# Performance work log

Measured on AMD Instinct MI355X. Metric: run time of the kernel, lower is better.

## Reference

```python
import jax, jax.numpy as jnp
import numpy as np
import math

B, C, H, W = 2, 256, 40, 40
NH, DK, DV, ERF = 8, 32, 32, 5
PAD = (ERF - 1) // 2
STRIDE = 2
HB, WB = 2 * H, 2 * W  # bottom (finer) level spatial size


def _unfold(x, k, p, s):
    # faithful torch F.unfold: x [B,C,Hi,Wi] -> [B, C*k*k, L], channel layout (c, kh, kw)
    Bn, Ci, Hi, Wi = x.shape
    xp = jnp.pad(x, ((0, 0), (0, 0), (p, p), (p, p)))
    Ho = (Hi + 2 * p - k) // s + 1
    Wo = (Wi + 2 * p - k) // s + 1
    rows = (jnp.arange(Ho) * s)[:, None] + jnp.arange(k)[None, :]  # [Ho,k]
    cols = (jnp.arange(Wo) * s)[:, None] + jnp.arange(k)[None, :]  # [Wo,k]
    pat = xp[:, :, rows[:, :, None, None], cols[None, None, :, :]]  # [B,C,Ho,k,Wo,k]
    pat = pat.transpose(0, 1, 3, 5, 2, 4)  # [B,C,k,k,Ho,Wo]
    return pat.reshape(Bn, Ci * k * k, Ho * Wo)


def _fold(y, out_hw, k, p, s):
    # faithful torch F.fold (scatter-add of overlapping patches)
    Bn, Ck2, L = y.shape
    Ci = Ck2 // (k * k)
    Hout, Wout = out_hw
    Ho = (Hout + 2 * p - k) // s + 1
    Wo = (Wout + 2 * p - k) // s + 1
    pat = y.reshape(Bn, Ci, k, k, Ho, Wo).transpose(0, 1, 4, 2, 5, 3)  # [B,C,Ho,k,Wo,k]
    rows = (jnp.arange(Ho) * s)[:, None] + jnp.arange(k)[None, :]
    cols = (jnp.arange(Wo) * s)[:, None] + jnp.arange(k)[None, :]
    out = jnp.zeros((Bn, Ci, Hout + 2 * p, Wout + 2 * p), y.dtype)
    out = out.at[:, :, rows[:, :, None, None], cols[None, None, :, :]].add(pat)
    return out[:, :, p:p + Hout, p:p + Wout]


def _conv1x1(x, w):
    # 1x1 conv, no bias; w [Cout, Cin]
    return jnp.einsum('oc,bchw->bohw', w, x)


def _plan_forward(top, bot, w_tk, w_tq, w_tv, w_bk, w_bq, w_bv, w_tf, w_bf):
    Bsz = top.shape[0]
    Hb, Wb = bot.shape[2], bot.shape[3]
    Bn = Bsz * NH  # heads merged into batch (head-major channel split)

    def top_proj(w, d):
        y = _conv1x1(top, w).reshape(Bn, d, H, W)
        return y.transpose(0, 2, 3, 1).reshape(Bn * H * W, 1, d)

    def bot_proj(w, d):
        y = _conv1x1(bot, w).reshape(Bn, d, Hb, Wb)
        u = _unfold(y, ERF, PAD, STRIDE)  # [Bn, d*e^2, H*W]
        # NOTE: original code reshapes (d*e^2) -> (e^2, d) directly, mixing
        # channel/position layout; we replicate that exactly.
        return u.transpose(0, 2, 1).reshape(Bn * H * W, ERF * ERF, d)

    K = jnp.concatenate([top_proj(w_tk, DK), bot_proj(w_bk, DK)], axis=1)  # [N,n,dk]
    Q = jnp.concatenate([top_proj(w_tq, DK), bot_proj(w_bq, DK)], axis=1)
    V = jnp.concatenate([top_proj(w_tv, DV), bot_proj(w_bv, DV)], axis=1)  # [N,n,dv]

    # weight[i,j] = key_i . query_j / sqrt(dk)  (no softmax)
    att = jnp.einsum('nid,njd->nij', K, Q) / math.sqrt(DK)
    out = jnp.einsum('nij,njv->niv', att, V)  # [N, n, dv]

    top_ret = out[:, 0, :].reshape(Bn, H, W, DV).transpose(0, 3, 1, 2)
    top_ret = top_ret.reshape(Bsz, NH * DV, H, W)

    bot_flat = out[:, 1:, :].reshape(Bn, H * W, ERF * ERF * DV).transpose(0, 2, 1)
    bot_ret = _fold(bot_flat, (Hb, Wb), ERF, PAD, STRIDE)  # [Bn, DV, Hb, Wb]
    bot_ret = bot_ret.reshape(Bsz, NH * DV, Hb, Wb)

    return _conv1x1(top_ret, w_tf), _conv1x1(bot_ret, w_bf)


def setup_inputs() -> dict:
    key = jax.random.key(0)
    ks = jax.random.split(key, 10)
    std = 0.01
    return {
        'top_feat': jax.random.normal(ks[0], (B, C, H, W), jnp.float32),
        'bot_feat': jax.random.normal(ks[1], (B, C, HB, WB), jnp.float32),
        'w_top_key': jax.random.normal(ks[2], (NH * DK, C), jnp.float32) * std,
        'w_top_query': jax.random.normal(ks[3], (NH * DK, C), jnp.float32) * std,
        'w_top_value': jax.random.normal(ks[4], (NH * DV, C), jnp.float32) * std,
        'w_bot_key': jax.random.normal(ks[5], (NH * DK, C), jnp.float32) * std,
        'w_bot_query': jax.random.normal(ks[6], (NH * DK, C), jnp.float32) * std,
        'w_bot_value': jax.random.normal(ks[7], (NH * DV, C), jnp.float32) * std,
        'w_top_fuse': jax.random.normal(ks[8], (C, NH * DV), jnp.float32) * std,
        'w_bot_fuse': jax.random.normal(ks[9], (C, NH * DV), jnp.float32) * std,
    }


def reference(top_feat, bot_feat, w_top_key, w_top_query, w_top_value,
              w_bot_key, w_bot_query, w_bot_value, w_top_fuse, w_bot_fuse):
    return _plan_forward(top_feat, bot_feat, w_top_key, w_top_query, w_top_value,
                         w_bot_key, w_bot_query, w_bot_value, w_top_fuse, w_bot_fuse)
```

## Files before the change

kernel.cpp:

```cpp
#include <hip/hip_runtime.h>

#define NB    2
#define NCH   256
#define HH    40
#define WW    40
#define HWT   1600
#define HBs   80
#define WBs   80
#define HWB   6400
#define NHD   8
#define BN    16

#define OFF_PTOP 0
#define OFF_PBOT 2457600
#define OFF_TR   12288000
#define OFF_BA   13107200
#define OFF_ATT  16384000
#define WS_NEED_DENSE  (36864000ULL * 4ULL)

__global__ __launch_bounds__(256) void proj_gemm(
    const float* __restrict__ X,
    const float* __restrict__ Wk,
    const float* __restrict__ Wq,
    const float* __restrict__ Wv,
    float* __restrict__ P,
    int npos)
{
  __shared__ float As[16][64];
  __shared__ float Bs[16][64];
  const int tid  = threadIdx.x;
  const int b    = blockIdx.z;
  const int oc0  = blockIdx.y * 64;
  const int pos0 = blockIdx.x * 64;
  const int tx   = tid & 15;
  const int ty   = tid >> 4;
  const int kqv  = oc0 >> 8;
  const int ocr  = oc0 & 255;
  const float* Wsel = (kqv == 0) ? Wk : ((kqv == 1) ? Wq : Wv);
  const float* Xb   = X + (size_t)b * NCH * npos;

  const int la_r = tid >> 2;
  const int la_c = (tid & 3) * 4;
  const int lb_r = tid >> 4;
  const int lb_c = (tid & 15) * 4;

  float acc[4][4];
#pragma unroll
  for (int i = 0; i < 4; ++i)
#pragma unroll
    for (int j = 0; j < 4; ++j) acc[i][j] = 0.f;

  for (int kt = 0; kt < 256; kt += 16) {
    float4 av = *(const float4*)&Wsel[(size_t)(ocr + la_r) * 256 + kt + la_c];
    float4 bv = *(const float4*)&Xb[(size_t)(kt + lb_r) * npos + pos0 + lb_c];
    __syncthreads();
    As[la_c + 0][la_r] = av.x;
    As[la_c + 1][la_r] = av.y;
    As[la_c + 2][la_r] = av.z;
    As[la_c + 3][la_r] = av.w;
    *(float4*)&Bs[lb_r][lb_c] = bv;
    __syncthreads();
#pragma unroll
    for (int kk = 0; kk < 16; ++kk) {
      float a[4], bb[4];
      *(float4*)a  = *(const float4*)&As[kk][tx * 4];
      *(float4*)bb = *(const float4*)&Bs[kk][ty * 4];
#pragma unroll
      for (int i = 0; i < 4; ++i)
#pragma unroll
        for (int j = 0; j < 4; ++j) acc[i][j] += a[i] * bb[j];
    }
  }

  const int ocl  = oc0 + tx * 4;
  const int hd   = ocl & 255;
  const int head = hd >> 5;
  const int d0   = hd & 31;
  const int bh   = b * NHD + head;
  float* Pb = P + (size_t)(kqv * BN + bh) * npos * 32;
#pragma unroll
  for (int j = 0; j < 4; ++j) {
    const int pos = pos0 + ty * 4 + j;
    *(float4*)&Pb[(size_t)pos * 32 + d0] =
        make_float4(acc[0][j], acc[1][j], acc[2][j], acc[3][j]);
  }
}

__device__ __forceinline__ void stage_rows(
    float* dst,
    const float* __restrict__ Ptopr,
    const float* __restrict__ Pbotp,
    int ho, int wo, int v, float scl)
{
  dst[v] = Ptopr[v] * scl;
#pragma unroll
  for (int p = 0; p < 25; ++p) {
    const int ki = p / 5, kj = p % 5;
    const int hb = 2 * ho - 2 + ki;
    const int wb = 2 * wo - 2 + kj;
    float val = 0.f;
    if (hb >= 0 && hb < HBs && wb >= 0 && wb < WBs)
      val = Pbotp[(size_t)(hb * WBs + wb) * 32 + v] * scl;
    dst[32 + v * 25 + p] = val;
  }
}

__global__ __launch_bounds__(256, 3) void attn_dense(
    const float* __restrict__ Ptop,
    const float* __restrict__ Pbot,
    float* __restrict__ TR,
    float* __restrict__ AttOut)
{
  __shared__ float SQ[8][832];
  __shared__ float SV[8][832];

  const int tid  = threadIdx.x;
  const int widx = tid >> 6;
  const int lane = tid & 63;
  const int nsub = lane >> 5;
  const int v    = lane & 31;
  const int slot = widx * 2 + nsub;
  const int n    = (blockIdx.x * 4 + widx) * 2 + nsub;
  const int b    = n / (NHD * HWT);
  const int head = (n / HWT) % NHD;
  const int hw   = n % HWT;
  const int ho   = hw / WW, wo = hw % WW;
  const int bh   = b * NHD + head;
  const float scale = 0.17677669529663687f;

  float* SQs = &SQ[slot][0];
  float* SVs = &SV[slot][0];

  stage_rows(SQs, Ptop + ((size_t)(1 * BN + bh) * HWT + hw) * 32,
             Pbot + (size_t)(1 * BN + bh) * HWB * 32, ho, wo, v, scale);
  stage_rows(SVs, Ptop + ((size_t)(2 * BN + bh) * HWT + hw) * 32,
             Pbot + (size_t)(2 * BN + bh) * HWB * 32, ho, wo, v, 1.f);

  float m[32];
#pragma unroll
  for (int x = 0; x < 32; ++x) m[x] = 0.f;

#pragma unroll 2
  for (int j = 0; j < 26; ++j) {
    const float vv = SVs[j * 32 + v];
    const float* qr = &SQs[j * 32];
#pragma unroll
    for (int c = 0; c < 8; ++c) {
      float4 t = *(const float4*)&qr[c * 4];
      m[c * 4 + 0] += t.x * vv;
      m[c * 4 + 1] += t.y * vv;
      m[c * 4 + 2] += t.z * vv;
      m[c * 4 + 3] += t.w * vv;
    }
  }

  stage_rows(SQs, Ptop + ((size_t)(0 * BN + bh) * HWT + hw) * 32,
             Pbot + (size_t)(0 * BN + bh) * HWB * 32, ho, wo, v, 1.f);

  float* TRn = TR + ((size_t)(b * HWT + hw)) * 256 + head * 32;
#pragma unroll 2
  for (int i = 0; i < 26; ++i) {
    const float* kr = &SQs[i * 32];
    float s0 = 0.f, s1 = 0.f, s2 = 0.f, s3 = 0.f;
#pragma unroll
    for (int c = 0; c < 8; ++c) {
      float4 t = *(const float4*)&kr[c * 4];
      s0 += t.x * m[c * 4 + 0];
      s1 += t.y * m[c * 4 + 1];
      s2 += t.z * m[c * 4 + 2];
      s3 += t.w * m[c * 4 + 3];
    }
    const float o = (s0 + s1) + (s2 + s3);
    if (i == 0) TRn[v] = o;
    else        SVs[(i - 1) * 32 + v] = o;
  }

  float* AOn = AttOut + (size_t)n * 800;
#pragma unroll 5
  for (int j = 0; j < 25; ++j)
    AOn[j * 32 + v] = SVs[v * 25 + j];
}

__global__ __launch_bounds__(256) void fold_gather(
    const float* __restrict__ AttOut,
    float* __restrict__ BA)
{
  const int t    = blockIdx.x * 256 + threadIdx.x;
  const int dq   = (t & 7) * 4;
  const int head = (t >> 3) & 7;
  const int pw   = t >> 6;
  const int pix  = pw % HWB;
  const int b    = pw / HWB;
  const int hb   = pix / WBs, wb = pix % WBs;

  const float* A = AttOut + (size_t)(b * NHD + head) * HWT * 800;
  float4 s = make_float4(0.f, 0.f, 0.f, 0.f);
  for (int ki = (hb & 1); ki < 5; ki += 2) {
    const int ho = (hb + 2 - ki) >> 1;
    if (ho < 0 || ho >= HH) continue;
    for (int kj = (wb & 1); kj < 5; kj += 2) {
      const int wo = (wb + 2 - kj) >> 1;
      if (wo < 0 || wo >= WW) continue;
      const float4 a4 = *(const float4*)&A[(size_t)(ho * WW + wo) * 800 +
                                           (ki * 5 + kj) * 32 + dq];
      s.x += a4.x; s.y += a4.y; s.z += a4.z; s.w += a4.w;
    }
  }
  *(float4*)&BA[(size_t)pw * 256 + head * 32 + dq] = s;
}

__global__ __launch_bounds__(256) void attn_atomic(
    const float* __restrict__ Ptop,
    const float* __restrict__ Pbot,
    float* __restrict__ TR,
    float* __restrict__ BA)
{
  __shared__ float SQ[8][832];
  __shared__ float SV[8][832];

  const int tid  = threadIdx.x;
  const int widx = tid >> 6;
  const int lane = tid & 63;
  const int nsub = lane >> 5;
  const int v    = lane & 31;
  const int slot = widx * 2 + nsub;
  const int n    = (blockIdx.x * 4 + widx) * 2 + nsub;
  const int b    = n / (NHD * HWT);
  const int head = (n / HWT) % NHD;
  const int hw   = n % HWT;
  const int ho   = hw / WW, wo = hw % WW;
  const int bh   = b * NHD + head;
  const float scale = 0.17677669529663687f;

  float* SQs = &SQ[slot][0];
  float* SVs = &SV[slot][0];

  stage_rows(SQs, Ptop + ((size_t)(1 * BN + bh) * HWT + hw) * 32,
             Pbot + (size_t)(1 * BN + bh) * HWB * 32, ho, wo, v, scale);
  stage_rows(SVs, Ptop + ((size_t)(2 * BN + bh) * HWT + hw) * 32,
             Pbot + (size_t)(2 * BN + bh) * HWB * 32, ho, wo, v, 1.f);

  float m[32];
#pragma unroll
  for (int x = 0; x < 32; ++x) m[x] = 0.f;

#pragma unroll 2
  for (int j = 0; j < 26; ++j) {
    const float vv = SVs[j * 32 + v];
    const float* qr = &SQs[j * 32];
#pragma unroll
    for (int c = 0; c < 8; ++c) {
      float4 t = *(const float4*)&qr[c * 4];
      m[c * 4 + 0] += t.x * vv;
      m[c * 4 + 1] += t.y * vv;
      m[c * 4 + 2] += t.z * vv;
      m[c * 4 + 3] += t.w * vv;
    }
  }

  stage_rows(SQs, Ptop + ((size_t)(0 * BN + bh) * HWT + hw) * 32,
             Pbot + (size_t)(0 * BN + bh) * HWB * 32, ho, wo, v, 1.f);

  for (int i = 0; i < 26; ++i) {
    const float* kr = &SQs[i * 32];
    float s0 = 0.f, s1 = 0.f, s2 = 0.f, s3 = 0.f;
#pragma unroll
    for (int c = 0; c < 8; ++c) {
      float4 t = *(const float4*)&kr[c * 4];
      s0 += t.x * m[c * 4 + 0];
      s1 += t.y * m[c * 4 + 1];
      s2 += t.z * m[c * 4 + 2];
      s3 += t.w * m[c * 4 + 3];
    }
    const float o = (s0 + s1) + (s2 + s3);
    if (i == 0) {
      TR[((size_t)(b * HWT + hw)) * 256 + head * 32 + v] = o;
    } else {
      const int flat = (i - 1) * 32 + v;
      const int dd = flat / 25;
      const int p  = flat % 25;
      const int ki = p / 5, kj = p % 5;
      const int hb = 2 * ho - 2 + ki;
      const int wb = 2 * wo - 2 + kj;
      if (hb >= 0 && hb < HBs && wb >= 0 && wb < WBs)
        atomicAdd(&BA[((size_t)(b * HWB + hb * WBs + wb)) * 256 + head * 32 + dd], o);
    }
  }
}

__global__ __launch_bounds__(256) void fuse_gemm(
    const float* __restrict__ Xp,
    const float* __restrict__ Wf,
    float* __restrict__ Out,
    int npos)
{
  __shared__ float As[16][64];
  __shared__ float Bs[16][64];
  const int tid  = threadIdx.x;
  const int b    = blockIdx.z;
  const int co0  = blockIdx.y * 64;
  const int pos0 = blockIdx.x * 64;
  const int tx   = tid & 15;
  const int ty   = tid >> 4;
  const float* Xb = Xp + (size_t)b * npos * 256;

  const int la_r = tid >> 2;
  const int la_c = (tid & 3) * 4;

  float acc[4][4];
#pragma unroll
  for (int i = 0; i < 4; ++i)
#pragma unroll
    for (int j = 0; j < 4; ++j) acc[i][j] = 0.f;

  for (int kt = 0; kt < 256; kt += 16) {
    float4 av = *(const float4*)&Wf[(size_t)(co0 + la_r) * 256 + kt + la_c];
    float4 bv = *(const float4*)&Xb[(size_t)(pos0 + la_r) * 256 + kt + la_c];
    __syncthreads();
    As[la_c + 0][la_r] = av.x;
    As[la_c + 1][la_r] = av.y;
    As[la_c + 2][la_r] = av.z;
    As[la_c + 3][la_r] = av.w;
    Bs[la_c + 0][la_r] = bv.x;
    Bs[la_c + 1][la_r] = bv.y;
    Bs[la_c + 2][la_r] = bv.z;
    Bs[la_c + 3][la_r] = bv.w;
    __syncthreads();
#pragma unroll
    for (int kk = 0; kk < 16; ++kk) {
      float a[4], bb[4];
      *(float4*)a  = *(const float4*)&As[kk][ty * 4];
      *(float4*)bb = *(const float4*)&Bs[kk][tx * 4];
#pragma unroll
      for (int i = 0; i < 4; ++i)
#pragma unroll
        for (int j = 0; j < 4; ++j) acc[i][j] += a[i] * bb[j];
    }
  }

  float* Ob = Out + (size_t)b * NCH * npos;
#pragma unroll
  for (int i = 0; i < 4; ++i) {
    const int co = co0 + ty * 4 + i;
    *(float4*)&Ob[(size_t)co * npos + pos0 + tx * 4] =
        make_float4(acc[i][0], acc[i][1], acc[i][2], acc[i][3]);
  }
}

extern "C" void kernel_launch(void* const* d_in, const int* in_sizes, int n_in,
                              void* d_out, int out_size, void* d_ws, size_t ws_size,
                              hipStream_t stream) {
  (void)in_sizes; (void)n_in; (void)out_size;
  const float* top = (const float*)d_in[0];
  const float* bot = (const float*)d_in[1];
  const float* wtk = (const float*)d_in[2];
  const float* wtq = (const float*)d_in[3];
  const float* wtv = (const float*)d_in[4];
  const float* wbk = (const float*)d_in[5];
  const float* wbq = (const float*)d_in[6];
  const float* wbv = (const float*)d_in[7];
  const float* wtf = (const float*)d_in[8];
  const float* wbf = (const float*)d_in[9];

  float* ws   = (float*)d_ws;
  float* Ptop = ws + OFF_PTOP;
  float* Pbot = ws + OFF_PBOT;
  float* TR   = ws + OFF_TR;
  float* BA   = ws + OFF_BA;
  float* Att  = ws + OFF_ATT;

  proj_gemm<<<dim3(HWT / 64, 12, NB), 256, 0, stream>>>(top, wtk, wtq, wtv, Ptop, HWT);
  proj_gemm<<<dim3(HWB / 64, 12, NB), 256, 0, stream>>>(bot, wbk, wbq, wbv, Pbot, HWB);

  if (ws_size >= WS_NEED_DENSE) {
    attn_dense<<<dim3(25600 / 8), 256, 0, stream>>>(Ptop, Pbot, TR, Att);
    fold_gather<<<dim3((NB * NHD * HWB * 8) / 256), 256, 0, stream>>>(Att, BA);
  } else {
    hipMemsetAsync(BA, 0, (size_t)NB * HWB * 256 * sizeof(float), stream);
    attn_atomic<<<dim3(25600 / 8), 256, 0, stream>>>(Ptop, Pbot, TR, BA);
  }

  fuse_gemm<<<dim3(HWT / 64, 4, NB), 256, 0, stream>>>(TR, wtf, (float*)d_out, HWT);
  fuse_gemm<<<dim3(HWB / 64, 4, NB), 256, 0, stream>>>(BA, wbf, (float*)d_out + (size_t)NB * NCH * HWT, HWB);
}
```

Baseline: 366.1 us.

## Use 128x128 register-tiled GEMMs for bottom level and slim attention LDS

Adds proj_gemm128 and fuse_gemm128 kernels using 128x128 tiles with 8x8 per-thread accumulators for the large bottom-level projection and fuse GEMMs. This raises arithmetic intensity and cuts shared-memory traffic per FLOP. attn_dense also drops its second shared buffer by holding the V column in registers, and raises its occupancy hint from 3 to 5 blocks. The bigger register footprint may lower occupancy in the GEMMs, and fewer blocks launch.

```diff
diff --git a/kernel.cpp b/kernel.cpp
--- a/kernel.cpp
+++ b/kernel.cpp
@@ -86,6 +86,86 @@
   }
 }
 
+__global__ __launch_bounds__(256) void proj_gemm128(
+    const float* __restrict__ X,
+    const float* __restrict__ Wk,
+    const float* __restrict__ Wq,
+    const float* __restrict__ Wv,
+    float* __restrict__ P,
+    int npos)
+{
+  __shared__ float As[16][128];
+  __shared__ float Bs[16][128];
+  const int tid  = threadIdx.x;
+  const int b    = blockIdx.z;
+  const int oc0  = blockIdx.y * 128;
+  const int pos0 = blockIdx.x * 128;
+  const int kqv  = oc0 >> 8;
+  const int ocr  = oc0 & 255;
+  const float* Wsel = (kqv == 0) ? Wk : ((kqv == 1) ? Wq : Wv);
+  const float* Xb   = X + (size_t)b * NCH * npos;
+
+  const int a_oc = tid & 127;
+  const int a_k  = (tid >> 7) * 8;
+  const int b_k  = tid >> 5;
+  const int b_p  = (tid & 31) * 4;
+
+  const int tx = (tid & 15) * 8;
+  const int ty = (tid >> 4) * 8;
+
+  float acc[8][8];
+#pragma unroll
+  for (int i = 0; i < 8; ++i)
+#pragma unroll
+    for (int j = 0; j < 8; ++j) acc[i][j] = 0.f;
+
+  for (int kt = 0; kt < 256; kt += 16) {
+    const float* wrow = &Wsel[(size_t)(ocr + a_oc) * 256 + kt + a_k];
+    float4 a0 = *(const float4*)&wrow[0];
+    float4 a1 = *(const float4*)&wrow[4];
+    float4 c0 = *(const float4*)&Xb[(size_t)(kt + b_k) * npos + pos0 + b_p];
+    float4 c1 = *(const float4*)&Xb[(size_t)(kt + b_k + 8) * npos + pos0 + b_p];
+    __syncthreads();
+    As[a_k + 0][a_oc] = a0.x;
+    As[a_k + 1][a_oc] = a0.y;
+    As[a_k + 2][a_oc] = a0.z;
+    As[a_k + 3][a_oc] = a0.w;
+    As[a_k + 4][a_oc] = a1.x;
+    As[a_k + 5][a_oc] = a1.y;
+    As[a_k + 6][a_oc] = a1.z;
+    As[a_k + 7][a_oc] = a1.w;
+    *(float4*)&Bs[b_k][b_p]     = c0;
+    *(float4*)&Bs[b_k + 8][b_p] = c1;
+    __syncthreads();
+#pragma unroll
+    for (int kk = 0; kk < 16; ++kk) {
+      float a[8], bb[8];
+      *(float4*)&a[0]  = *(const float4*)&As[kk][tx];
+      *(float4*)&a[4]  = *(const float4*)&As[kk][tx + 4];
+      *(float4*)&bb[0] = *(const float4*)&Bs[kk][ty];
+      *(float4*)&bb[4] = *(const float4*)&Bs[kk][ty + 4];
+#pragma unroll
+      for (int i = 0; i < 8; ++i)
+#pragma unroll
+        for (int j = 0; j < 8; ++j) acc[i][j] += a[i] * bb[j];
+    }
+  }
+
+  const int hd0  = ocr + tx;
+  const int head = hd0 >> 5;
+  const int d0   = hd0 & 31;
+  const int bh   = b * NHD + head;
+  float* Pb = P + (size_t)(kqv * BN + bh) * npos * 32;
+#pragma unroll
+  for (int j = 0; j < 8; ++j) {
+    const size_t base = (size_t)(pos0 + ty + j) * 32 + d0;
+    *(float4*)&Pb[base] =
+        make_float4(acc[0][j], acc[1][j], acc[2][j], acc[3][j]);
+    *(float4*)&Pb[base + 4] =
+        make_float4(acc[4][j], acc[5][j], acc[6][j], acc[7][j]);
+  }
+}
+
 __device__ __forceinline__ void stage_rows(
     float* dst,
     const float* __restrict__ Ptopr,
@@ -105,14 +185,13 @@
   }
 }
 
-__global__ __launch_bounds__(256, 3) void attn_dense(
+__global__ __launch_bounds__(256, 5) void attn_dense(
     const float* __restrict__ Ptop,
     const float* __restrict__ Pbot,
     float* __restrict__ TR,
     float* __restrict__ AttOut)
 {
-  __shared__ float SQ[8][832];
-  __shared__ float SV[8][832];
+  __shared__ float SM[8][832];
 
   const int tid  = threadIdx.x;
   const int widx = tid >> 6;
@@ -128,22 +207,37 @@
   const int bh   = b * NHD + head;
   const float scale = 0.17677669529663687f;
 
-  float* SQs = &SQ[slot][0];
-  float* SVs = &SV[slot][0];
-
-  stage_rows(SQs, Ptop + ((size_t)(1 * BN + bh) * HWT + hw) * 32,
+  float* SMs = &SM[slot][0];
+
+  const float* PbotV = Pbot + (size_t)(2 * BN + bh) * HWB * 32;
+  float vcol[26];
+  vcol[0] = Ptop[((size_t)(2 * BN + bh) * HWT + hw) * 32 + v];
+#pragma unroll
+  for (int a = 0; a < 25; ++a) {
+    const int flat = a * 32 + v;
+    const int d  = (flat * 1311) >> 15;
+    const int p  = flat - d * 25;
+    const int ki = (p * 13) >> 6;
+    const int kj = p - ki * 5;
+    const int hb = 2 * ho - 2 + ki;
+    const int wb = 2 * wo - 2 + kj;
+    float val = 0.f;
+    if (hb >= 0 && hb < HBs && wb >= 0 && wb < WBs)
+      val = PbotV[(size_t)(hb * WBs + wb) * 32 + d];
+    vcol[1 + a] = val;
+  }
+
+  stage_rows(SMs, Ptop + ((size_t)(1 * BN + bh) * HWT + hw) * 32,
              Pbot + (size_t)(1 * BN + bh) * HWB * 32, ho, wo, v, scale);
-  stage_rows(SVs, Ptop + ((size_t)(2 * BN + bh) * HWT + hw) * 32,
-             Pbot + (size_t)(2 * BN + bh) * HWB * 32, ho, wo, v, 1.f);
 
   float m[32];
 #pragma unroll
   for (int x = 0; x < 32; ++x) m[x] = 0.f;
 
-#pragma unroll 2
+#pragma unroll
   for (int j = 0; j < 26; ++j) {
-    const float vv = SVs[j * 32 + v];
-    const float* qr = &SQs[j * 32];
+    const float vv = vcol[j];
+    const float* qr = &SMs[j * 32];
 #pragma unroll
     for (int c = 0; c < 8; ++c) {
       float4 t = *(const float4*)&qr[c * 4];
@@ -154,13 +248,13 @@
     }
   }
 
-  stage_rows(SQs, Ptop + ((size_t)(0 * BN + bh) * HWT + hw) * 32,
+  stage_rows(SMs, Ptop + ((size_t)(0 * BN + bh) * HWT + hw) * 32,
              Pbot + (size_t)(0 * BN + bh) * HWB * 32, ho, wo, v, 1.f);
 
   float* TRn = TR + ((size_t)(b * HWT + hw)) * 256 + head * 32;
 #pragma unroll 2
   for (int i = 0; i < 26; ++i) {
-    const float* kr = &SQs[i * 32];
+    const float* kr = &SMs[i * 32];
     float s0 = 0.f, s1 = 0.f, s2 = 0.f, s3 = 0.f;
 #pragma unroll
     for (int c = 0; c < 8; ++c) {
@@ -172,13 +266,13 @@
     }
     const float o = (s0 + s1) + (s2 + s3);
     if (i == 0) TRn[v] = o;
-    else        SVs[(i - 1) * 32 + v] = o;
+    else        SMs[i * 32 + v] = o;
   }
 
   float* AOn = AttOut + (size_t)n * 800;
 #pragma unroll 5
   for (int j = 0; j < 25; ++j)
-    AOn[j * 32 + v] = SVs[v * 25 + j];
+    AOn[j * 32 + v] = SMs[32 + v * 25 + j];
 }
 
 __global__ __launch_bounds__(256) void fold_gather(
@@ -344,6 +438,82 @@
     const int co = co0 + ty * 4 + i;
     *(float4*)&Ob[(size_t)co * npos + pos0 + tx * 4] =
         make_float4(acc[i][0], acc[i][1], acc[i][2], acc[i][3]);
+  }
+}
+
+__global__ __launch_bounds__(256) void fuse_gemm128(
+    const float* __restrict__ Xp,
+    const float* __restrict__ Wf,
+    float* __restrict__ Out,
+    int npos)
+{
+  __shared__ float As[16][128];
+  __shared__ float Bs[16][128];
+  const int tid  = threadIdx.x;
+  const int b    = blockIdx.z;
+  const int co0  = blockIdx.y * 128;
+  const int pos0 = blockIdx.x * 128;
+  const float* Xb = Xp + (size_t)b * npos * 256;
+
+  const int a_co  = tid & 127;
+  const int a_k   = (tid >> 7) * 8;
+  const int b_pos = tid & 127;
+  const int b_k   = (tid >> 7) * 8;
+
+  const int px = (tid & 15) * 8;
+  const int cy = (tid >> 4) * 8;
+
+  float acc[8][8];
+#pragma unroll
+  for (int i = 0; i < 8; ++i)
+#pragma unroll
+    for (int j = 0; j < 8; ++j) acc[i][j] = 0.f;
+
+  for (int kt = 0; kt < 256; kt += 16) {
+    const float* wrow = &Wf[(size_t)(co0 + a_co) * 256 + kt + a_k];
+    float4 a0 = *(const float4*)&wrow[0];
+    float4 a1 = *(const float4*)&wrow[4];
+    const float* xrow = &Xb[(size_t)(pos0 + b_pos) * 256 + kt + b_k];
+    float4 c0 = *(const float4*)&xrow[0];
+    float4 c1 = *(const float4*)&xrow[4];
+    __syncthreads();
+    As[a_k + 0][a_co] = a0.x;
+    As[a_k + 1][a_co] = a0.y;
+    As[a_k + 2][a_co] = a0.z;
+    As[a_k + 3][a_co] = a0.w;
+    As[a_k + 4][a_co] = a1.x;
+    As[a_k + 5][a_co] = a1.y;
+    As[a_k + 6][a_co] = a1.z;
+    As[a_k + 7][a_co] = a1.w;
+    Bs[b_k + 0][b_pos] = c0.x;
+    Bs[b_k + 1][b_pos] = c0.y;
+    Bs[b_k + 2][b_pos] = c0.z;
+    Bs[b_k + 3][b_pos] = c0.w;
+    Bs[b_k + 4][b_pos] = c1.x;
+    Bs[b_k + 5][b_pos] = c1.y;
+    Bs[b_k + 6][b_pos] = c1.z;
+    Bs[b_k + 7][b_pos] = c1.w;
+    __syncthreads();
+#pragma unroll
+    for (int kk = 0; kk < 16; ++kk) {
+      float a[8], bb[8];
+      *(float4*)&a[0]  = *(const float4*)&As[kk][cy];
+      *(float4*)&a[4]  = *(const float4*)&As[kk][cy + 4];
+      *(float4*)&bb[0] = *(const float4*)&Bs[kk][px];
+      *(float4*)&bb[4] = *(const float4*)&Bs[kk][px + 4];
+#pragma unroll
+      for (int i = 0; i < 8; ++i)
+#pragma unroll
+        for (int j = 0; j < 8; ++j) acc[i][j] += a[i] * bb[j];
+    }
+  }
+
+  float* Ob = Out + (size_t)b * NCH * npos;
+#pragma unroll
+  for (int i = 0; i < 8; ++i) {
+    const size_t base = (size_t)(co0 + cy + i) * npos + pos0 + px;
+    *(float4*)&Ob[base]     = make_float4(acc[i][0], acc[i][1], acc[i][2], acc[i][3]);
+    *(float4*)&Ob[base + 4] = make_float4(acc[i][4], acc[i][5], acc[i][6], acc[i][7]);
   }
 }
 
@@ -370,7 +540,7 @@
   float* Att  = ws + OFF_ATT;
 
   proj_gemm<<<dim3(HWT / 64, 12, NB), 256, 0, stream>>>(top, wtk, wtq, wtv, Ptop, HWT);
-  proj_gemm<<<dim3(HWB / 64, 12, NB), 256, 0, stream>>>(bot, wbk, wbq, wbv, Pbot, HWB);
+  proj_gemm128<<<dim3(HWB / 128, 6, NB), 256, 0, stream>>>(bot, wbk, wbq, wbv, Pbot, HWB);
 
   if (ws_size >= WS_NEED_DENSE) {
     attn_dense<<<dim3(25600 / 8), 256, 0, stream>>>(Ptop, Pbot, TR, Att);
@@ -381,5 +551,5 @@
   }
 
   fuse_gemm<<<dim3(HWT / 64, 4, NB), 256, 0, stream>>>(TR, wtf, (float*)d_out, HWT);
-  fuse_gemm<<<dim3(HWB / 64, 4, NB), 256, 0, stream>>>(BA, wbf, (float*)d_out + (size_t)NB * NCH * HWT, HWB);
-}
+  fuse_gemm128<<<dim3(HWB / 128, 2, NB), 256, 0, stream>>>(BA, wbf, (float*)d_out + (size_t)NB * NCH * HWT, HWB);
+}
```

After: 1.458 ms. 298% more time.
